# Performance work log

Measured on AMD Instinct MI355X. Metric: run time of the kernel, lower is better.

## Reference

```python
import jax, jax.numpy as jnp
import numpy as np


def setup_inputs() -> dict:
    key = jax.random.key(0)
    W = jax.random.normal(key, (64, 16, 128, 128), dtype=jnp.float32)
    return {"W": W, "num_iters": 5}


def reference(W, num_iters):
    """Newton-Schulz iterative matrix inverse: X_{k+1} = X_k (2I - W X_k).

    Init: X_0 = W^T / (||W||_1 * ||W||_inf), the classical convergent start.
    W: [..., N, N] batched square matrices.
    """
    n = W.shape[-1]
    absW = jnp.abs(W)
    norm1 = jnp.max(jnp.sum(absW, axis=-2), axis=-1)    # max abs column sum
    norminf = jnp.max(jnp.sum(absW, axis=-1), axis=-1)  # max abs row sum
    scale = (norm1 * norminf)[..., None, None]
    X = jnp.swapaxes(W, -1, -2) / scale
    two_I = 2.0 * jnp.eye(n, dtype=W.dtype)
    for _ in range(num_iters):
        X = jnp.matmul(X, two_I - jnp.matmul(W, X))
    return X
```

## Files before the change

kernel.cpp:

```cpp
#include <hip/hip_runtime.h>


#define NN 128

typedef __attribute__((ext_vector_type(8))) short bf16x8;
typedef __attribute__((ext_vector_type(16))) float f32x16;
typedef __attribute__((ext_vector_type(4))) float f32x4;
typedef __attribute__((ext_vector_type(4))) unsigned short us4;

#define WRM_OFF   0
#define XRM_OFF   32768
#define XCM_OFF   65536
#define SCR_OFF   98304
#define STAGE_OFF 98304
#define RED_OFF   32768
#define LDS_BYTES 163840

__device__ __forceinline__ unsigned short f2bf(float f) {
  unsigned u = __float_as_uint(f);
  return (unsigned short)((u + 0x7FFFu + ((u >> 16) & 1u)) >> 16);
}
__device__ __forceinline__ float bf2f(unsigned short h) {
  return __uint_as_float(((unsigned)h) << 16);
}
__device__ __forceinline__ f32x16 zero16() {
  f32x16 z;
#pragma unroll
  for (int i = 0; i < 16; ++i) z[i] = 0.0f;
  return z;
}
__device__ __forceinline__ int swz8(int R, int k0) {
  return R * 128 + (((k0 >> 3) ^ (R & 7)) << 3);
}
__device__ __forceinline__ int swz4(int R, int c0) {
  return R * 128 + ((((c0 >> 3) ^ (R & 7)) << 3) | (c0 & 7));
}
__device__ __forceinline__ int swz1(int R, int c) {
  return R * 128 + ((((c >> 3) ^ (R & 7)) << 3) | (c & 7));
}

__global__ void __launch_bounds__(1024)
ns_inverse_kernel(const float* __restrict__ Wglob, const int* __restrict__ nIt,
                  float* __restrict__ outglob) {
  extern __shared__ char lds[];
  unsigned short* wrm = (unsigned short*)(lds + WRM_OFF);
  unsigned short* xrm = (unsigned short*)(lds + XRM_OFF);
  unsigned short* xcm = (unsigned short*)(lds + XCM_OFF);
  unsigned short* scr = (unsigned short*)(lds + SCR_OFF);
  float* stage = (float*)(lds + STAGE_OFF);
  float* red   = (float*)(lds + RED_OFF);

  const int b = blockIdx.x;
  const float* Wg = Wglob + (size_t)b * (NN * NN);
  float* outg = outglob + (size_t)b * (NN * NN);
  const int t = threadIdx.x;
  const int lane = t & 63;
  const int wv = t >> 6;
  const int l31 = lane & 31;
  const int half = lane >> 5;
  const int s = wv & 3;
  const int v = wv >> 2;
  const int niters = nIt[0];

  {
    const f32x4* src = (const f32x4*)Wg;
    f32x4* dst = (f32x4*)stage;
#pragma unroll
    for (int i = 0; i < 4; ++i) dst[t + 1024 * i] = src[t + 1024 * i];
  }
  __syncthreads();

  if (t < 128) {
    float ssum = 0.f;
    for (int jj = 0; jj < NN; ++jj) { int j = (jj + t) & 127; ssum += fabsf(stage[t * NN + j]); }
    red[t] = ssum;
  } else if (t < 256) {
    int c = t - 128;
    float ssum = 0.f;
    for (int i = 0; i < NN; ++i) ssum += fabsf(stage[i * NN + c]);
    red[128 + c] = ssum;
  }
  __syncthreads();
  float ninf = 0.f, n1 = 0.f;
  for (int i = 0; i < 128; ++i) {
    ninf = fmaxf(ninf, red[i]);
    n1   = fmaxf(n1,   red[128 + i]);
  }
  const float scale = 1.0f / (n1 * ninf);
  __syncthreads();

  {
    const int r = t >> 3;
    const int c0 = (t & 7) * 16;
#pragma unroll
    for (int h = 0; h < 4; ++h) {
      f32x4 a = *(const f32x4*)(stage + r * NN + c0 + 4 * h);
      us4 hw, hx;
#pragma unroll
      for (int i = 0; i < 4; ++i) {
        hw[i] = f2bf(a[i]);
        hx[i] = f2bf(a[i] * scale);
      }
      *(us4*)(wrm + swz4(r, c0 + 4 * h)) = hw;
      *(us4*)(xcm + swz4(r, c0 + 4 * h)) = hx;
    }
  }
  {
    const int r = t & 127;
    const int kc = (t >> 7) * 16;
#pragma unroll
    for (int j4 = 0; j4 < 4; ++j4) {
      int c0 = kc + 4 * j4;
      us4 h4;
#pragma unroll
      for (int i = 0; i < 4; ++i) h4[i] = f2bf(stage[(c0 + i) * NN + r] * scale);
      *(us4*)(xrm + swz4(r, c0)) = h4;
    }
  }
  __syncthreads();

  const int pX = 32 * s + l31;
  const int rv = 32 * v + l31;
  for (int it = 0; it < niters; ++it) {
    const bool last = (it == niters - 1);

    {
      f32x16 tt = zero16();
#pragma unroll
      for (int ks = 0; ks < 8; ++ks) {
        int k0 = ks * 16 + half * 8;
        bf16x8 av = *(const bf16x8*)(wrm + swz8(pX, k0));
        bf16x8 bv = *(const bf16x8*)(xcm + swz8(rv, k0));
        tt = __builtin_amdgcn_mfma_f32_32x32x16_bf16(av, bv, tt, 0, 0, 0);
      }
#pragma unroll
      for (int q = 0; q < 4; ++q) {
        us4 h4;
#pragma unroll
        for (int i = 0; i < 4; ++i) h4[i] = f2bf(tt[4 * q + i]);
        *(us4*)(scr + swz4(rv, 32 * s + 8 * q + 4 * half)) = h4;
      }
    }
    __syncthreads();

    f32x16 acc = zero16();
#pragma unroll
    for (int ks = 0; ks < 8; ++ks) {
      int k0 = ks * 16 + half * 8;
      bf16x8 av = *(const bf16x8*)(scr + swz8(rv, k0));
      bf16x8 bv = *(const bf16x8*)(xrm + swz8(pX, k0));
      acc = __builtin_amdgcn_mfma_f32_32x32x16_bf16(av, bv, acc, 0, 0, 0);
    }
    __syncthreads();

#pragma unroll
    for (int q = 0; q < 4; ++q) {
      int c0m = 32 * v + 8 * q + 4 * half;
      int offr = swz4(pX, c0m);
      us4 xh4 = *(const us4*)(xrm + offr);
      f32x4 vv;
#pragma unroll
      for (int i = 0; i < 4; ++i)
        vv[i] = 2.0f * bf2f(xh4[i]) - acc[4 * q + i];
      if (last) {
        *(f32x4*)(outg + pX * NN + c0m) = vv;
      } else {
        us4 h4;
#pragma unroll
        for (int i = 0; i < 4; ++i) {
          unsigned short hh = f2bf(vv[i]);
          h4[i] = hh;
          xcm[swz1(c0m + i, pX)] = hh;
        }
        *(us4*)(xrm + offr) = h4;
      }
    }
    __syncthreads();
  }
}

extern "C" void kernel_launch(void* const* d_in, const int* in_sizes, int n_in,
                              void* d_out, int out_size, void* d_ws, size_t ws_size,
                              hipStream_t stream) {
  const float* W = (const float*)d_in[0];
  const int* nIt = (const int*)d_in[1];
  float* out = (float*)d_out;
  const int nmat = in_sizes[0] / (NN * NN);

  hipFuncSetAttribute((const void*)ns_inverse_kernel,
                      hipFuncAttributeMaxDynamicSharedMemorySize, LDS_BYTES);
  ns_inverse_kernel<<<nmat, 1024, LDS_BYTES, stream>>>(W, nIt, out);
}
```

Measured before the change: 203.9 us.

## Hold W fragments in registers and prefetch X before the barrier

W's bf16 MFMA A-fragments are built once from the fp32 staging buffer and kept in registers across all iterations, so the separate W buffer in LDS goes away and LDS per block shrinks from 160KB to 128KB. The X row-major fragments for the second matmul are loaded before the barrier, overlapping those LDS reads with the sync. The swizzle XOR changes from 8 to 16 chunk positions to reduce bank conflicts. These changes add register pressure at 1024 threads per block, which could cause spills.

```diff
diff --git a/kernel.cpp b/kernel.cpp
--- a/kernel.cpp
+++ b/kernel.cpp
@@ -8,13 +8,12 @@
 typedef __attribute__((ext_vector_type(4))) float f32x4;
 typedef __attribute__((ext_vector_type(4))) unsigned short us4;
 
-#define WRM_OFF   0
-#define XRM_OFF   32768
-#define XCM_OFF   65536
-#define SCR_OFF   98304
-#define STAGE_OFF 98304
-#define RED_OFF   32768
-#define LDS_BYTES 163840
+#define XRM_OFF   0
+#define XCM_OFF   32768
+#define SCR_OFF   65536
+#define STAGE_OFF 65536
+#define RED_OFF   0
+#define LDS_BYTES 131072
 
 __device__ __forceinline__ unsigned short f2bf(float f) {
   unsigned u = __float_as_uint(f);
@@ -30,20 +29,19 @@
   return z;
 }
 __device__ __forceinline__ int swz8(int R, int k0) {
-  return R * 128 + (((k0 >> 3) ^ (R & 7)) << 3);
+  return R * 128 + (((k0 >> 3) ^ (R & 15)) << 3);
 }
 __device__ __forceinline__ int swz4(int R, int c0) {
-  return R * 128 + ((((c0 >> 3) ^ (R & 7)) << 3) | (c0 & 7));
+  return R * 128 + ((((c0 >> 3) ^ (R & 15)) << 3) | (c0 & 7));
 }
 __device__ __forceinline__ int swz1(int R, int c) {
-  return R * 128 + ((((c >> 3) ^ (R & 7)) << 3) | (c & 7));
+  return R * 128 + ((((c >> 3) ^ (R & 15)) << 3) | (c & 7));
 }
 
 __global__ void __launch_bounds__(1024)
 ns_inverse_kernel(const float* __restrict__ Wglob, const int* __restrict__ nIt,
                   float* __restrict__ outglob) {
   extern __shared__ char lds[];
-  unsigned short* wrm = (unsigned short*)(lds + WRM_OFF);
   unsigned short* xrm = (unsigned short*)(lds + XRM_OFF);
   unsigned short* xcm = (unsigned short*)(lds + XCM_OFF);
   unsigned short* scr = (unsigned short*)(lds + SCR_OFF);
@@ -89,19 +87,31 @@
   const float scale = 1.0f / (n1 * ninf);
   __syncthreads();
 
+  const int pX = 32 * s + l31;
+  bf16x8 wfrag[8];
+#pragma unroll
+  for (int ks = 0; ks < 8; ++ks) {
+    const float* src = stage + pX * NN + 16 * ks + 8 * half;
+    f32x4 f0 = *(const f32x4*)(src);
+    f32x4 f1 = *(const f32x4*)(src + 4);
+    bf16x8 wb;
+#pragma unroll
+    for (int e = 0; e < 4; ++e) {
+      wb[e]     = (short)f2bf(f0[e]);
+      wb[4 + e] = (short)f2bf(f1[e]);
+    }
+    wfrag[ks] = wb;
+  }
+
   {
     const int r = t >> 3;
     const int c0 = (t & 7) * 16;
 #pragma unroll
     for (int h = 0; h < 4; ++h) {
       f32x4 a = *(const f32x4*)(stage + r * NN + c0 + 4 * h);
-      us4 hw, hx;
-#pragma unroll
-      for (int i = 0; i < 4; ++i) {
-        hw[i] = f2bf(a[i]);
-        hx[i] = f2bf(a[i] * scale);
-      }
-      *(us4*)(wrm + swz4(r, c0 + 4 * h)) = hw;
+      us4 hx;
+#pragma unroll
+      for (int i = 0; i < 4; ++i) hx[i] = f2bf(a[i] * scale);
       *(us4*)(xcm + swz4(r, c0 + 4 * h)) = hx;
     }
   }
@@ -119,19 +129,23 @@
   }
   __syncthreads();
 
-  const int pX = 32 * s + l31;
   const int rv = 32 * v + l31;
   for (int it = 0; it < niters; ++it) {
     const bool last = (it == niters - 1);
 
+    bf16x8 xb[8];
     {
       f32x16 tt = zero16();
 #pragma unroll
       for (int ks = 0; ks < 8; ++ks) {
         int k0 = ks * 16 + half * 8;
-        bf16x8 av = *(const bf16x8*)(wrm + swz8(pX, k0));
         bf16x8 bv = *(const bf16x8*)(xcm + swz8(rv, k0));
-        tt = __builtin_amdgcn_mfma_f32_32x32x16_bf16(av, bv, tt, 0, 0, 0);
+        tt = __builtin_amdgcn_mfma_f32_32x32x16_bf16(wfrag[ks], bv, tt, 0, 0, 0);
+      }
+#pragma unroll
+      for (int ks = 0; ks < 8; ++ks) {
+        int k0 = ks * 16 + half * 8;
+        xb[ks] = *(const bf16x8*)(xrm + swz8(pX, k0));
       }
 #pragma unroll
       for (int q = 0; q < 4; ++q) {
@@ -148,8 +162,7 @@
     for (int ks = 0; ks < 8; ++ks) {
       int k0 = ks * 16 + half * 8;
       bf16x8 av = *(const bf16x8*)(scr + swz8(rv, k0));
-      bf16x8 bv = *(const bf16x8*)(xrm + swz8(pX, k0));
-      acc = __builtin_amdgcn_mfma_f32_32x32x16_bf16(av, bv, acc, 0, 0, 0);
+      acc = __builtin_amdgcn_mfma_f32_32x32x16_bf16(av, xb[ks], acc, 0, 0, 0);
     }
     __syncthreads();
 
```

Result: slower. 238.7 us (+17.1%).
